# Kernel optimization log

Hardware: AMD Instinct MI355X
Metric: run time of the kernel (lower is better)

## Reference

```python
import jax, jax.numpy as jnp
import numpy as np

D_MODEL, D_EDGE, D_STRUCT = 128, 64, 8
N, E, B = 50000, 800000, 1

def _lin(key, din, dout):
    kw, kb = jax.random.split(key)
    s = 1.0 / np.sqrt(din)
    return (jax.random.uniform(kw, (din, dout), jnp.float32, -s, s),
            jax.random.uniform(kb, (dout,), jnp.float32, -s, s))

def setup_inputs() -> dict:
    key = jax.random.key(0)
    ks = jax.random.split(key, 16)
    H = jax.random.normal(ks[0], (B, N, D_MODEL), jnp.float32)
    xyz = jax.random.normal(ks[1], (B, N, 3), jnp.float32)
    edge_index = jax.random.randint(ks[2], (2, E), 0, N, jnp.int64)
    edge_struct = jax.random.normal(ks[3], (E, D_STRUCT), jnp.float32)
    edge_rest_lengths = jax.random.uniform(ks[4], (E,), jnp.float32)
    We1, be1 = _lin(ks[5], 2 * D_MODEL + 2 + D_STRUCT, D_EDGE)
    We2, be2 = _lin(ks[6], D_EDGE, D_EDGE)
    Wg1, bg1 = _lin(ks[7], 2 + D_STRUCT, 32)
    Wg2, bg2 = _lin(ks[8], 32, 1)
    Wn1, bn1 = _lin(ks[9], D_MODEL + D_EDGE, 2 * D_MODEL)
    Wn2, bn2 = _lin(ks[10], 2 * D_MODEL, D_MODEL)
    ln_g = jnp.ones((D_MODEL,), jnp.float32)
    ln_b = jnp.zeros((D_MODEL,), jnp.float32)
    return dict(H=H, xyz=xyz, edge_index=edge_index, edge_struct=edge_struct,
                edge_rest_lengths=edge_rest_lengths,
                We1=We1, be1=be1, We2=We2, be2=be2,
                Wg1=Wg1, bg1=bg1, Wg2=Wg2, bg2=bg2,
                Wn1=Wn1, bn1=bn1, Wn2=Wn2, bn2=bn2,
                ln_g=ln_g, ln_b=ln_b)

def reference(H, xyz, edge_index, edge_struct, edge_rest_lengths,
              We1, be1, We2, be2, Wg1, bg1, Wg2, bg2,
              Wn1, bn1, Wn2, bn2, ln_g, ln_b):
    Bn, Nn, d = H.shape
    i, j = edge_index[0], edge_index[1]
    # edge geometry
    diff = xyz[:, i, :] - xyz[:, j, :]                      # (B,E,3)
    dist2 = jnp.sum(diff * diff, axis=-1, keepdims=True)    # (B,E,1)
    dist = jnp.sqrt(dist2 + 1e-9)
    rest = edge_rest_lengths.reshape(1, -1, 1)
    delta = (dist - rest) / (rest + 1e-9)
    struct = jnp.broadcast_to(edge_struct[None], (Bn, edge_struct.shape[0], edge_struct.shape[1]))
    # edge message MLP
    Hi, Hj = H[:, i, :], H[:, j, :]
    e_in = jnp.concatenate([Hi, Hj, dist2, delta, struct], axis=-1)  # (B,E,2d+2+ds)
    e = jax.nn.silu(e_in @ We1 + be1)
    e_msg = jax.nn.silu(e @ We2 + be2)                       # (B,E,d_edge)
    # gate
    g_in = jnp.concatenate([dist2, delta, struct], axis=-1)
    g = jax.nn.sigmoid(jax.nn.silu(g_in @ Wg1 + bg1) @ Wg2 + bg2)  # (B,E,1)
    e_msg = e_msg * g
    # scatter-add aggregate to destination node i
    agg = jnp.zeros((Bn, Nn, e_msg.shape[-1]), H.dtype).at[:, i, :].add(e_msg)
    # node MLP (dropout is identity at eval) + residual + LayerNorm
    n_in = jnp.concatenate([H, agg], axis=-1)
    upd = jax.nn.silu(n_in @ Wn1 + bn1) @ Wn2 + bn2
    x = H + upd
    mu = jnp.mean(x, axis=-1, keepdims=True)
    var = jnp.mean((x - mu) ** 2, axis=-1, keepdims=True)
    return (x - mu) / jnp.sqrt(var + 1e-5) * ln_g + ln_b
```

## Files before the change

kernel.cpp:

```cpp
#include <hip/hip_runtime.h>
#include <stdint.h>

#define N_NODES 50000
#define N_EDGES 800000
#define NODE_TILES 782

#define SE   72
#define SW2  72
#define SPQ  136
#define SN1  216
#define SN2  280
#define ATS  40

#define EC_GRID 962
#define EC_CHUNK 13

#define SCAN_B 98

typedef short bf16x8 __attribute__((ext_vector_type(8)));
typedef short short4v __attribute__((ext_vector_type(4)));
typedef unsigned short ushort8 __attribute__((ext_vector_type(8)));
typedef unsigned int uint4v __attribute__((ext_vector_type(4)));
typedef float f32x4  __attribute__((ext_vector_type(4)));

static __device__ __forceinline__ unsigned short f2bf(float f) {
  unsigned int x = __float_as_uint(f);
  unsigned int r = (x + 0x7fffu + ((x >> 16) & 1u)) >> 16;
  return (unsigned short)r;
}
static __device__ __forceinline__ float bf2f(unsigned short u) {
  return __uint_as_float(((unsigned int)u) << 16);
}
static __device__ __forceinline__ float silu_f(float x) {
  return x * __builtin_amdgcn_rcpf(1.0f + __expf(-x));
}
static __device__ __forceinline__ float sigmoid_f(float x) {
  return __builtin_amdgcn_rcpf(1.0f + __expf(-x));
}
static __device__ __forceinline__ unsigned int cvt_pk_bf16(float lo, float hi) {
  unsigned int r;
  asm("v_cvt_pk_bf16_f32 %0, %1, %2" : "=v"(r) : "v"(lo), "v"(hi));
  return r;
}
static __device__ __forceinline__ bf16x8 pack8(float4 u, float4 v) {
  bf16x8 w;
  w[0] = (short)f2bf(u.x); w[1] = (short)f2bf(u.y);
  w[2] = (short)f2bf(u.z); w[3] = (short)f2bf(u.w);
  w[4] = (short)f2bf(v.x); w[5] = (short)f2bf(v.y);
  w[6] = (short)f2bf(v.z); w[7] = (short)f2bf(v.w);
  return w;
}

__global__ void prep_hist(
    const int* __restrict__ eidx,
    const float* __restrict__ We1, const float* __restrict__ be1,
    const float* __restrict__ We2,
    const float* __restrict__ Wn1, const float* __restrict__ Wn2,
    unsigned short* __restrict__ WpqT, unsigned short* __restrict__ We2T,
    unsigned short* __restrict__ Wn1T, unsigned short* __restrict__ Wn2T,
    unsigned short* __restrict__ WrT,
    int* __restrict__ cnt)
{
  const int gid = blockIdx.x * 256 + threadIdx.x;
  const int gsz = gridDim.x * 256;
  for (int i = gid; i < 128 * SPQ; i += gsz) {
    int n = i / SPQ, k = i % SPQ;
    unsigned short v = 0;
    if (k < 128) v = (n < 64) ? f2bf(We1[k * 64 + n]) : f2bf(We1[(128 + k) * 64 + (n - 64)]);
    WpqT[i] = v;
  }
  for (int i = gid; i < 64 * SW2; i += gsz) {
    int n = i / SW2, k = i % SW2;
    We2T[i] = (k < 64) ? f2bf(We2[k * 64 + n]) : (unsigned short)0;
  }
  for (int i = gid; i < 256 * SN1; i += gsz) {
    int n = i / SN1, k = i % SN1;
    Wn1T[i] = (k < 192) ? f2bf(Wn1[k * 256 + n]) : (unsigned short)0;
  }
  for (int i = gid; i < 128 * SN2; i += gsz) {
    int n = i / SN2, k = i % SN2;
    Wn2T[i] = (k < 256) ? f2bf(Wn2[k * 128 + n]) : (unsigned short)0;
  }
  for (int i = gid; i < 64 * 32; i += gsz) {
    int n = i >> 5, k = i & 31;
    float v = 0.f;
    if (k < 2)       v = We1[256 * 64 + n];
    else if (k < 4)  v = We1[257 * 64 + n];
    else if (k < 12) v = We1[(258 + (k - 4)) * 64 + n];
    else if (k == 12) v = be1[n];
    else if (k == 13) { float w = We1[256 * 64 + n]; v = w - bf2f(f2bf(w)); }
    else if (k == 14) { float w = We1[257 * 64 + n]; v = w - bf2f(f2bf(w)); }
    else if (k == 15) { float w = be1[n];            v = w - bf2f(f2bf(w)); }
    WrT[i] = (k < 16) ? f2bf(v) : (unsigned short)0;
  }
  if (gid < N_EDGES) atomicAdd(&cnt[eidx[gid]], 1);
}

__global__ __launch_bounds__(512) void scan_local(
    const int* __restrict__ cnt, int* __restrict__ rowptr,
    int* __restrict__ bsum)
{
  __shared__ int wsum[8], woff[8];
  const int t = threadIdx.x;
  const int idx = blockIdx.x * 512 + t;
  const int lane = t & 63, wid = t >> 6;
  int c = (idx < N_NODES) ? cnt[idx] : 0;
  int v = c;
  #pragma unroll
  for (int o = 1; o < 64; o <<= 1) {
    int u = __shfl_up(v, o);
    if (lane >= o) v += u;
  }
  if (lane == 63) wsum[wid] = v;
  __syncthreads();
  if (t == 0) {
    int a = 0;
    #pragma unroll
    for (int w = 0; w < 8; ++w) { woff[w] = a; a += wsum[w]; }
    bsum[blockIdx.x] = a;
  }
  __syncthreads();
  if (idx < N_NODES) rowptr[idx] = woff[wid] + (v - c);
}

__global__ __launch_bounds__(128) void scan_mid(
    const int* __restrict__ bsum, int* __restrict__ boff)
{
  __shared__ int ws[2];
  const int t = threadIdx.x;
  const int lane = t & 63, wid = t >> 6;
  int c = (t < SCAN_B) ? bsum[t] : 0;
  int v = c;
  #pragma unroll
  for (int o = 1; o < 64; o <<= 1) {
    int u = __shfl_up(v, o);
    if (lane >= o) v += u;
  }
  if (lane == 63) ws[wid] = v;
  __syncthreads();
  int add = (wid == 1) ? ws[0] : 0;
  if (t < SCAN_B) boff[t] = add + (v - c);
}

__global__ __launch_bounds__(512) void scan_add(
    const int* __restrict__ rowptr, const int* __restrict__ boff,
    int* __restrict__ cursor, float4* __restrict__ agg)
{
  const int idx = blockIdx.x * 512 + threadIdx.x;
  if (idx < N_NODES) cursor[idx] = rowptr[idx] + boff[blockIdx.x];
  if (idx < 50048) {
    float4 z = make_float4(0.f, 0.f, 0.f, 0.f);
    float4* p = agg + (long)idx * 16;
    #pragma unroll
    for (int k = 0; k < 16; ++k) p[k] = z;
  }
}

__global__ void fill_reorder(
    const int* __restrict__ eidx, const float* __restrict__ xyz,
    const float* __restrict__ estruct, const float* __restrict__ erest,
    int* __restrict__ cursor,
    const float* __restrict__ Wg1, const float* __restrict__ bg1,
    const float* __restrict__ Wg2, const float* __restrict__ bg2,
    unsigned short* __restrict__ rec)
{
  int e = blockIdx.x * 256 + threadIdx.x;
  if (e >= N_EDGES) return;
  int i = eidx[e], j = eidx[N_EDGES + e];
  float dx = xyz[i * 3 + 0] - xyz[j * 3 + 0];
  float dy = xyz[i * 3 + 1] - xyz[j * 3 + 1];
  float dz = xyz[i * 3 + 2] - xyz[j * 3 + 2];
  float d2 = dx * dx + dy * dy + dz * dz;
  float dist = sqrtf(d2 + 1e-9f);
  float rest = erest[e];
  float dl = (dist - rest) / (rest + 1e-9f);
  float4 s0 = *(const float4*)&estruct[e * 8];
  float4 s1 = *(const float4*)&estruct[e * 8 + 4];
  float st[8] = {s0.x, s0.y, s0.z, s0.w, s1.x, s1.y, s1.z, s1.w};
  float gsum = 0.f;
  #pragma unroll
  for (int h = 0; h < 32; ++h) {
    float a = bg1[h] + d2 * Wg1[0 * 32 + h] + dl * Wg1[1 * 32 + h];
    #pragma unroll
    for (int c = 0; c < 8; ++c) a += st[c] * Wg1[(2 + c) * 32 + h];
    gsum += silu_f(a) * Wg2[h];
  }
  float g = sigmoid_f(gsum + bg2[0]);

  unsigned short d2h = f2bf(d2);
  unsigned short d2l = f2bf(d2 - bf2f(d2h));
  unsigned short dlh = f2bf(dl);
  unsigned short dll = f2bf(dl - bf2f(dlh));

  ushort8 w0;
  w0[0] = d2h; w0[1] = d2l; w0[2] = dlh; w0[3] = dll;
  w0[4] = f2bf(st[0]); w0[5] = f2bf(st[1]); w0[6] = f2bf(st[2]); w0[7] = f2bf(st[3]);
  uint4v w1;
  w1[0] = (unsigned int)f2bf(st[4]) | ((unsigned int)f2bf(st[5]) << 16);
  w1[1] = (unsigned int)f2bf(st[6]) | ((unsigned int)f2bf(st[7]) << 16);
  w1[2] = __float_as_uint(g);
  w1[3] = (unsigned int)i | ((unsigned int)j << 16);

  int pos = atomicAdd(&cursor[i], 1);
  unsigned short* dst = rec + (long)pos * 16;
  *(uint4v*)dst = *(uint4v*)&w0;
  *(uint4v*)(dst + 8) = w1;
}

__global__ __launch_bounds__(256, 4) void pq_kernel(
    const float* __restrict__ H, const unsigned short* __restrict__ WpqT,
    unsigned short* __restrict__ P, unsigned short* __restrict__ Q,
    unsigned short* __restrict__ Hbf)
{
  __shared__ unsigned short Ws[128 * SPQ];

  const int tid  = threadIdx.x;
  const int lane = tid & 63;
  const int wv   = tid >> 6;
  const int lr   = lane & 15;
  const int lq   = lane >> 4;
  const int n0   = blockIdx.x * 64;
  const int m0   = wv * 16;

  for (int i = tid * 8; i < 128 * SPQ; i += 256 * 8)
    *(bf16x8*)&Ws[i] = *(const bf16x8*)&WpqT[i];
  __syncthreads();

  const int rowa = n0 + m0 + lr;
  const int rowc = rowa < N_NODES ? rowa : N_NODES - 1;

  f32x4 zero4 = {0.f, 0.f, 0.f, 0.f};
  f32x4 acc[8];
  #pragma unroll
  for (int f = 0; f < 8; ++f) acc[f] = zero4;

  #pragma unroll
  for (int s = 0; s < 4; ++s) {
    int kb = s * 32 + lq * 8;
    const float* p = H + (long)rowc * 128 + kb;
    float4 u = *(const float4*)p;
    float4 v = *(const float4*)(p + 4);
    bf16x8 a = pack8(u, v);
    *(bf16x8*)&Hbf[(long)rowa * 128 + kb] = a;
    #pragma unroll
    for (int f = 0; f < 8; ++f) {
      bf16x8 b = *(const bf16x8*)&Ws[(f * 16 + lr) * SPQ + kb];
      acc[f] = __builtin_amdgcn_mfma_f32_16x16x32_bf16(a, b, acc[f], 0, 0, 0);
    }
  }
  #pragma unroll
  for (int f = 0; f < 8; ++f) {
    #pragma unroll
    for (int r = 0; r < 4; ++r) {
      int node = n0 + m0 + lq * 4 + r;
      if (node < N_NODES) {
        if (f < 4) P[(long)node * 64 + f * 16 + lr] = f2bf(acc[f][r]);
        else       Q[(long)node * 64 + (f - 4) * 16 + lr] = f2bf(acc[f][r]);
      }
    }
  }
}

__global__ __launch_bounds__(256, 4) void edge_compute(
    const unsigned short* __restrict__ P, const unsigned short* __restrict__ Q,
    const unsigned short* __restrict__ rec,
    const unsigned short* __restrict__ We2T, const float* __restrict__ be2,
    const unsigned short* __restrict__ WrT,
    float* __restrict__ agg)
{
  __shared__ unsigned short W2s[64 * SW2];
  __shared__ unsigned short Es [4 * 16 * SE];
  __shared__ unsigned short At [4 * 16 * ATS];

  const int tid  = threadIdx.x;
  const int lane = tid & 63;
  const int wv   = tid >> 6;
  const int lr   = lane & 15;
  const int lq   = lane >> 4;

  for (int i = tid * 8; i < 64 * SW2; i += 256 * 8)
    *(bf16x8*)&W2s[i] = *(const bf16x8*)&We2T[i];

  unsigned short* Es_w = &Es[wv * 16 * SE];
  unsigned short* At_w = &At[wv * 16 * ATS];

  if (lane < 16) {
    ushort8 z;
    #pragma unroll
    for (int c = 0; c < 8; ++c) z[c] = 0;
    *(ushort8*)&At_w[lane * ATS + 16] = z;
    *(ushort8*)&At_w[lane * ATS + 24] = z;
  }

  bf16x8 aWr[4];
  float bias2[4][4];
  #pragma unroll
  for (int f = 0; f < 4; ++f) {
    aWr[f] = *(const bf16x8*)&WrT[(f * 16 + lr) * 32 + lq * 8];
    #pragma unroll
    for (int r = 0; r < 4; ++r) bias2[f][r] = be2[f * 16 + lq * 4 + r];
  }
  __syncthreads();

  const int n_tiles = N_EDGES / 16;
  const int wid = blockIdx.x * 4 + wv;
  const int t0 = wid * EC_CHUNK;
  const int t1 = (t0 + EC_CHUNK < n_tiles) ? (t0 + EC_CHUNK) : n_tiles;
  if (t0 >= n_tiles) return;

  f32x4 zero4 = {0.f, 0.f, 0.f, 0.f};
  int   cur_node;
  {
    int ij0 = *(const int*)(rec + (long)t0 * 16 * 16 + 14);
    cur_node = ij0 & 0xffff;
  }
  float acc        = 0.f;
  bool  use_atomic = true;

  for (int tile = t0; tile < t1; ++tile) {
    const int s0 = tile * 16;

    const unsigned short* rp = rec + (long)(s0 + lr) * 16;
    ushort8 ra = *(const ushort8*)rp;
    uint4   rb = *(const uint4*)(rp + 8);
    float g     = __uint_as_float(rb.z);
    int   inode = (int)(rb.w & 0xffff);
    int   jnode = (int)((rb.w >> 16) & 0xffff);

    if (lane < 16) {
      ushort8 w1;
      w1[0] = (unsigned short)(rb.x & 0xffff);
      w1[1] = (unsigned short)(rb.x >> 16);
      w1[2] = (unsigned short)(rb.y & 0xffff);
      w1[3] = (unsigned short)(rb.y >> 16);
      w1[4] = 0x3F80u; w1[5] = (unsigned short)ra[0];
      w1[6] = (unsigned short)ra[2]; w1[7] = 0x3F80u;
      *(ushort8*)&At_w[lane * ATS]     = ra;
      *(ushort8*)&At_w[lane * ATS + 8] = w1;
    }

    bf16x8 bA = *(const bf16x8*)&At_w[lr * ATS + lq * 8];
    f32x4 acc1[4];
    #pragma unroll
    for (int f = 0; f < 4; ++f)
      acc1[f] = __builtin_amdgcn_mfma_f32_16x16x32_bf16(aWr[f], bA, zero4, 0, 0, 0);

    const unsigned short* Pb = P + (long)inode * 64;
    const unsigned short* Qb = Q + (long)jnode * 64;
    #pragma unroll
    for (int f = 0; f < 4; ++f) {
      short4v pv = *(const short4v*)&Pb[f * 16 + lq * 4];
      short4v qv = *(const short4v*)&Qb[f * 16 + lq * 4];
      float v0 = silu_f(bf2f((unsigned short)pv[0]) + bf2f((unsigned short)qv[0]) + acc1[f][0]);
      float v1 = silu_f(bf2f((unsigned short)pv[1]) + bf2f((unsigned short)qv[1]) + acc1[f][1]);
      float v2 = silu_f(bf2f((unsigned short)pv[2]) + bf2f((unsigned short)qv[2]) + acc1[f][2]);
      float v3 = silu_f(bf2f((unsigned short)pv[3]) + bf2f((unsigned short)qv[3]) + acc1[f][3]);
      uint2 w;
      w.x = cvt_pk_bf16(v0, v1);
      w.y = cvt_pk_bf16(v2, v3);
      *(uint2*)&Es_w[lr * SE + f * 16 + lq * 4] = w;
    }

    f32x4 acc2[4];
    #pragma unroll
    for (int f = 0; f < 4; ++f) acc2[f] = zero4;
    #pragma unroll
    for (int s = 0; s < 2; ++s) {
      int kb = s * 32 + lq * 8;
      bf16x8 bE = *(const bf16x8*)&Es_w[lr * SE + kb];
      #pragma unroll
      for (int f = 0; f < 4; ++f) {
        bf16x8 aW = *(const bf16x8*)&W2s[(f * 16 + lr) * SW2 + kb];
        acc2[f] = __builtin_amdgcn_mfma_f32_16x16x32_bf16(aW, bE, acc2[f], 0, 0, 0);
      }
    }

    #pragma unroll
    for (int f = 0; f < 4; ++f) {
      float o0 = silu_f(acc2[f][0] + bias2[f][0]) * g;
      float o1 = silu_f(acc2[f][1] + bias2[f][1]) * g;
      float o2 = silu_f(acc2[f][2] + bias2[f][2]) * g;
      float o3 = silu_f(acc2[f][3] + bias2[f][3]) * g;
      uint2 w;
      w.x = cvt_pk_bf16(o0, o1);
      w.y = cvt_pk_bf16(o2, o3);
      *(uint2*)&Es_w[lr * SE + f * 16 + lq * 4] = w;
    }

    float mv[16];
    #pragma unroll
    for (int e = 0; e < 16; ++e) mv[e] = bf2f(Es_w[e * SE + lane]);

    int up = __shfl_up(inode, 1);
    unsigned long long bm = __ballot(inode != up);
    unsigned mask = (unsigned)bm & 0xFFFEu;
    int i0 = __builtin_amdgcn_readlane(inode, 0);
    if (i0 != cur_node) mask |= 1u;

    #pragma unroll
    for (int e = 0; e < 16; ++e) {
      if (mask & (1u << e)) {
        if (use_atomic) atomicAdd(&agg[(long)cur_node * 64 + lane], acc);
        else            agg[(long)cur_node * 64 + lane] = acc;
        use_atomic = false;
        cur_node = __builtin_amdgcn_readlane(inode, e);
        acc = 0.f;
      }
      acc += mv[e];
    }
  }
  atomicAdd(&agg[(long)cur_node * 64 + lane], acc);
}

__global__ __launch_bounds__(256, 2) void h1_kernel(
    const unsigned short* __restrict__ Hbf, const float* __restrict__ agg,
    const unsigned short* __restrict__ Wn1T, const float* __restrict__ bn1,
    unsigned short* __restrict__ h1)
{
  __shared__ unsigned short Wl[128 * SN1];

  const int tid  = threadIdx.x;
  const int lane = tid & 63;
  const int wv   = tid >> 6;
  const int lr   = lane & 15;
  const int lq   = lane >> 4;
  const int m0   = wv * 16;
  const int p    = blockIdx.x & 1;

  for (int i = tid * 8; i < 128 * SN1; i += 256 * 8)
    *(bf16x8*)&Wl[i] = *(const bf16x8*)&Wn1T[p * 128 * SN1 + i];
  __syncthreads();

  f32x4 zero4 = {0.f, 0.f, 0.f, 0.f};
  for (int t = blockIdx.x >> 1; t < NODE_TILES; t += 256) {
    const int n0 = t * 64;
    int rowa = n0 + m0 + lr;
    int rowc = rowa < N_NODES ? rowa : N_NODES - 1;

    f32x4 acc1[8];
    #pragma unroll
    for (int f = 0; f < 8; ++f) acc1[f] = zero4;
    #pragma unroll
    for (int s = 0; s < 6; ++s) {
      int kb = s * 32 + lq * 8;
      bf16x8 a;
      if (s < 4) {
        a = *(const bf16x8*)&Hbf[(long)rowa * 128 + kb];
      } else {
        const float* pp = agg + (long)rowc * 64 + (kb - 128);
        float4 u = *(const float4*)pp;
        float4 v = *(const float4*)(pp + 4);
        a = pack8(u, v);
      }
      #pragma unroll
      for (int f = 0; f < 8; ++f) {
        bf16x8 b = *(const bf16x8*)&Wl[(f * 16 + lr) * SN1 + kb];
        acc1[f] = __builtin_amdgcn_mfma_f32_16x16x32_bf16(a, b, acc1[f], 0, 0, 0);
      }
    }
    #pragma unroll
    for (int f = 0; f < 8; ++f) {
      int col = p * 128 + f * 16 + lr;
      float bias = bn1[col];
      #pragma unroll
      for (int r = 0; r < 4; ++r) {
        int node = n0 + m0 + lq * 4 + r;
        h1[(long)node * 256 + col] = f2bf(silu_f(acc1[f][r] + bias));
      }
    }
  }
}

__global__ __launch_bounds__(256, 2) void out_kernel(
    const float* __restrict__ H, const unsigned short* __restrict__ h1,
    const unsigned short* __restrict__ Wn2T, const float* __restrict__ bn2,
    const float* __restrict__ ln_g, const float* __restrict__ ln_b,
    float* __restrict__ out)
{
  __shared__ unsigned short Wl[128 * SN2];

  const int tid  = threadIdx.x;
  const int lane = tid & 63;
  const int wv   = tid >> 6;
  const int lr   = lane & 15;
  const int lq   = lane >> 4;
  const int m0   = wv * 16;

  for (int i = tid * 8; i < 128 * SN2; i += 256 * 8)
    *(bf16x8*)&Wl[i] = *(const bf16x8*)&Wn2T[i];
  __syncthreads();

  f32x4 zero4 = {0.f, 0.f, 0.f, 0.f};
  for (int t = blockIdx.x; t < NODE_TILES; t += 512) {
    const int n0 = t * 64;
    int rowa = n0 + m0 + lr;

    f32x4 acc2[8];
    #pragma unroll
    for (int f = 0; f < 8; ++f) acc2[f] = zero4;
    #pragma unroll
    for (int s = 0; s < 8; ++s) {
      int kb = s * 32 + lq * 8;
      bf16x8 a = *(const bf16x8*)&h1[(long)rowa * 256 + kb];
      #pragma unroll
      for (int f = 0; f < 8; ++f) {
        bf16x8 b = *(const bf16x8*)&Wl[(f * 16 + lr) * SN2 + kb];
        acc2[f] = __builtin_amdgcn_mfma_f32_16x16x32_bf16(a, b, acc2[f], 0, 0, 0);
      }
    }

    #pragma unroll
    for (int r = 0; r < 4; ++r) {
      int node = n0 + m0 + lq * 4 + r;
      int nc = node < N_NODES ? node : N_NODES - 1;
      float x[8];
      float sum = 0.f, sumsq = 0.f;
      #pragma unroll
      for (int f = 0; f < 8; ++f) {
        int n = f * 16 + lr;
        float u = acc2[f][r] + bn2[n];
        float xv = H[(long)nc * 128 + n] + u;
        x[f] = xv;
        sum += xv;
        sumsq += xv * xv;
      }
      #pragma unroll
      for (int o = 1; o < 16; o <<= 1) {
        sum   += __shfl_xor(sum, o);
        sumsq += __shfl_xor(sumsq, o);
      }
      float mu  = sum * (1.f / 128.f);
      float var = sumsq * (1.f / 128.f) - mu * mu;
      float rstd = rsqrtf(var + 1e-5f);
      if (node < N_NODES) {
        #pragma unroll
        for (int f = 0; f < 8; ++f) {
          int n = f * 16 + lr;
          out[(long)node * 128 + n] = (x[f] - mu) * rstd * ln_g[n] + ln_b[n];
        }
      }
    }
  }
}

extern "C" void kernel_launch(void* const* d_in, const int* in_sizes, int n_in,
                              void* d_out, int out_size, void* d_ws, size_t ws_size,
                              hipStream_t stream) {
  const float* H       = (const float*)d_in[0];
  const float* xyz     = (const float*)d_in[1];
  const int*   eidx    = (const int*)d_in[2];
  const float* estruct = (const float*)d_in[3];
  const float* erest   = (const float*)d_in[4];
  const float* We1     = (const float*)d_in[5];
  const float* be1     = (const float*)d_in[6];
  const float* We2     = (const float*)d_in[7];
  const float* be2     = (const float*)d_in[8];
  const float* Wg1     = (const float*)d_in[9];
  const float* bg1     = (const float*)d_in[10];
  const float* Wg2     = (const float*)d_in[11];
  const float* bg2     = (const float*)d_in[12];
  const float* Wn1     = (const float*)d_in[13];
  const float* bn1     = (const float*)d_in[14];
  const float* Wn2     = (const float*)d_in[15];
  const float* bn2     = (const float*)d_in[16];
  const float* ln_g    = (const float*)d_in[17];
  const float* ln_b    = (const float*)d_in[18];

  char* ws = (char*)d_ws;
  float*          agg    = (float*)(ws + 0);
  unsigned short* Hbf    = (unsigned short*)(ws + 12812288);
  unsigned short* rec    = (unsigned short*)(ws + 25624576);
  unsigned short* P      = (unsigned short*)(ws + 51224576);
  unsigned short* Qm     = (unsigned short*)(ws + 57624576);
  int*            cnt    = (int*)(ws + 64024576);
  int*            rowptr = (int*)(ws + 64224768);
  int*            cursor = (int*)(ws + 64424960);
  unsigned short* WpqT   = (unsigned short*)(ws + 64625152);
  unsigned short* We2T   = (unsigned short*)(ws + 64659968);
  unsigned short* Wn1T   = (unsigned short*)(ws + 64669184);
  unsigned short* Wn2T   = (unsigned short*)(ws + 64779776);
  unsigned short* WrT    = (unsigned short*)(ws + 64851456);
  int*            bsum   = (int*)(ws + 64855552);
  int*            boff   = (int*)(ws + 64856064);
  unsigned short* h1     = (unsigned short*)(ws + 64856576);
  float* out = (float*)d_out;

  hipMemsetAsync(cnt, 0, (size_t)N_NODES * sizeof(int), stream);

  hipLaunchKernelGGL(prep_hist, dim3(3125), dim3(256), 0, stream,
                     eidx, We1, be1, We2, Wn1, Wn2, WpqT, We2T, Wn1T, Wn2T, WrT, cnt);
  hipLaunchKernelGGL(scan_local, dim3(SCAN_B), dim3(512), 0, stream,
                     cnt, rowptr, bsum);
  hipLaunchKernelGGL(scan_mid, dim3(1), dim3(128), 0, stream,
                     bsum, boff);
  hipLaunchKernelGGL(scan_add, dim3(SCAN_B), dim3(512), 0, stream,
                     rowptr, boff, cursor, (float4*)agg);
  hipLaunchKernelGGL(fill_reorder, dim3(3125), dim3(256), 0, stream,
                     eidx, xyz, estruct, erest, cursor,
                     Wg1, bg1, Wg2, bg2, rec);
  hipLaunchKernelGGL(pq_kernel, dim3(NODE_TILES), dim3(256), 0, stream,
                     H, WpqT, P, Qm, Hbf);
  hipLaunchKernelGGL(edge_compute, dim3(EC_GRID), dim3(256), 0, stream,
                     P, Qm, rec, We2T, be2, WrT, agg);
  hipLaunchKernelGGL(h1_kernel, dim3(512), dim3(256), 0, stream,
                     Hbf, agg, Wn1T, bn1, h1);
  hipLaunchKernelGGL(out_kernel, dim3(512), dim3(256), 0, stream,
                     H, h1, Wn2T, bn2, ln_g, ln_b, out);
}
```

Measured before the change: 362.3 us.

## Drop CSR sort and fuse edge geometry and gate MLP into edge kernel

Removes the histogram, three-phase scan and reorder pass that sorted edges by destination node. Edge geometry, features and the gate MLP (now run on MFMA with bf16 weights) are computed inside the edge kernel. Aggregation switches from segmented register reduction to per-element float atomicAdd into agg. This removes several launches and the write and read of the 25 MB record buffer, but issues 64 atomics per edge to random nodes (about 51M atomics) and computes the gate in bf16, which loses precision.

```diff
diff --git a/kernel.cpp b/kernel.cpp
--- a/kernel.cpp
+++ b/kernel.cpp
@@ -14,8 +14,6 @@
 
 #define EC_GRID 962
 #define EC_CHUNK 13
-
-#define SCAN_B 98
 
 typedef short bf16x8 __attribute__((ext_vector_type(8)));
 typedef short short4v __attribute__((ext_vector_type(4)));
@@ -51,15 +49,14 @@
   return w;
 }
 
-__global__ void prep_hist(
-    const int* __restrict__ eidx,
+__global__ void prep_w(
     const float* __restrict__ We1, const float* __restrict__ be1,
     const float* __restrict__ We2,
     const float* __restrict__ Wn1, const float* __restrict__ Wn2,
+    const float* __restrict__ Wg1, const float* __restrict__ bg1,
     unsigned short* __restrict__ WpqT, unsigned short* __restrict__ We2T,
     unsigned short* __restrict__ Wn1T, unsigned short* __restrict__ Wn2T,
-    unsigned short* __restrict__ WrT,
-    int* __restrict__ cnt)
+    unsigned short* __restrict__ WrT,  unsigned short* __restrict__ WgT)
 {
   const int gid = blockIdx.x * 256 + threadIdx.x;
   const int gsz = gridDim.x * 256;
@@ -93,118 +90,15 @@
     else if (k == 15) { float w = be1[n];            v = w - bf2f(f2bf(w)); }
     WrT[i] = (k < 16) ? f2bf(v) : (unsigned short)0;
   }
-  if (gid < N_EDGES) atomicAdd(&cnt[eidx[gid]], 1);
-}
-
-__global__ __launch_bounds__(512) void scan_local(
-    const int* __restrict__ cnt, int* __restrict__ rowptr,
-    int* __restrict__ bsum)
-{
-  __shared__ int wsum[8], woff[8];
-  const int t = threadIdx.x;
-  const int idx = blockIdx.x * 512 + t;
-  const int lane = t & 63, wid = t >> 6;
-  int c = (idx < N_NODES) ? cnt[idx] : 0;
-  int v = c;
-  #pragma unroll
-  for (int o = 1; o < 64; o <<= 1) {
-    int u = __shfl_up(v, o);
-    if (lane >= o) v += u;
-  }
-  if (lane == 63) wsum[wid] = v;
-  __syncthreads();
-  if (t == 0) {
-    int a = 0;
-    #pragma unroll
-    for (int w = 0; w < 8; ++w) { woff[w] = a; a += wsum[w]; }
-    bsum[blockIdx.x] = a;
-  }
-  __syncthreads();
-  if (idx < N_NODES) rowptr[idx] = woff[wid] + (v - c);
-}
-
-__global__ __launch_bounds__(128) void scan_mid(
-    const int* __restrict__ bsum, int* __restrict__ boff)
-{
-  __shared__ int ws[2];
-  const int t = threadIdx.x;
-  const int lane = t & 63, wid = t >> 6;
-  int c = (t < SCAN_B) ? bsum[t] : 0;
-  int v = c;
-  #pragma unroll
-  for (int o = 1; o < 64; o <<= 1) {
-    int u = __shfl_up(v, o);
-    if (lane >= o) v += u;
-  }
-  if (lane == 63) ws[wid] = v;
-  __syncthreads();
-  int add = (wid == 1) ? ws[0] : 0;
-  if (t < SCAN_B) boff[t] = add + (v - c);
-}
-
-__global__ __launch_bounds__(512) void scan_add(
-    const int* __restrict__ rowptr, const int* __restrict__ boff,
-    int* __restrict__ cursor, float4* __restrict__ agg)
-{
-  const int idx = blockIdx.x * 512 + threadIdx.x;
-  if (idx < N_NODES) cursor[idx] = rowptr[idx] + boff[blockIdx.x];
-  if (idx < 50048) {
-    float4 z = make_float4(0.f, 0.f, 0.f, 0.f);
-    float4* p = agg + (long)idx * 16;
-    #pragma unroll
-    for (int k = 0; k < 16; ++k) p[k] = z;
-  }
-}
-
-__global__ void fill_reorder(
-    const int* __restrict__ eidx, const float* __restrict__ xyz,
-    const float* __restrict__ estruct, const float* __restrict__ erest,
-    int* __restrict__ cursor,
-    const float* __restrict__ Wg1, const float* __restrict__ bg1,
-    const float* __restrict__ Wg2, const float* __restrict__ bg2,
-    unsigned short* __restrict__ rec)
-{
-  int e = blockIdx.x * 256 + threadIdx.x;
-  if (e >= N_EDGES) return;
-  int i = eidx[e], j = eidx[N_EDGES + e];
-  float dx = xyz[i * 3 + 0] - xyz[j * 3 + 0];
-  float dy = xyz[i * 3 + 1] - xyz[j * 3 + 1];
-  float dz = xyz[i * 3 + 2] - xyz[j * 3 + 2];
-  float d2 = dx * dx + dy * dy + dz * dz;
-  float dist = sqrtf(d2 + 1e-9f);
-  float rest = erest[e];
-  float dl = (dist - rest) / (rest + 1e-9f);
-  float4 s0 = *(const float4*)&estruct[e * 8];
-  float4 s1 = *(const float4*)&estruct[e * 8 + 4];
-  float st[8] = {s0.x, s0.y, s0.z, s0.w, s1.x, s1.y, s1.z, s1.w};
-  float gsum = 0.f;
-  #pragma unroll
-  for (int h = 0; h < 32; ++h) {
-    float a = bg1[h] + d2 * Wg1[0 * 32 + h] + dl * Wg1[1 * 32 + h];
-    #pragma unroll
-    for (int c = 0; c < 8; ++c) a += st[c] * Wg1[(2 + c) * 32 + h];
-    gsum += silu_f(a) * Wg2[h];
-  }
-  float g = sigmoid_f(gsum + bg2[0]);
-
-  unsigned short d2h = f2bf(d2);
-  unsigned short d2l = f2bf(d2 - bf2f(d2h));
-  unsigned short dlh = f2bf(dl);
-  unsigned short dll = f2bf(dl - bf2f(dlh));
-
-  ushort8 w0;
-  w0[0] = d2h; w0[1] = d2l; w0[2] = dlh; w0[3] = dll;
-  w0[4] = f2bf(st[0]); w0[5] = f2bf(st[1]); w0[6] = f2bf(st[2]); w0[7] = f2bf(st[3]);
-  uint4v w1;
-  w1[0] = (unsigned int)f2bf(st[4]) | ((unsigned int)f2bf(st[5]) << 16);
-  w1[1] = (unsigned int)f2bf(st[6]) | ((unsigned int)f2bf(st[7]) << 16);
-  w1[2] = __float_as_uint(g);
-  w1[3] = (unsigned int)i | ((unsigned int)j << 16);
-
-  int pos = atomicAdd(&cursor[i], 1);
-  unsigned short* dst = rec + (long)pos * 16;
-  *(uint4v*)dst = *(uint4v*)&w0;
-  *(uint4v*)(dst + 8) = w1;
+  for (int i = gid; i < 32 * 32; i += gsz) {
+    int h = i >> 5, k = i & 31;
+    float v = 0.f;
+    if (k < 2)       v = Wg1[0 * 32 + h];
+    else if (k < 4)  v = Wg1[1 * 32 + h];
+    else if (k < 12) v = Wg1[(2 + (k - 4)) * 32 + h];
+    else if (k == 12) v = bg1[h];
+    WgT[i] = f2bf(v);
+  }
 }
 
 __global__ __launch_bounds__(256, 4) void pq_kernel(
@@ -261,11 +155,13 @@
   }
 }
 
-__global__ __launch_bounds__(256, 4) void edge_compute(
+__global__ __launch_bounds__(256, 4) void edge_all(
+    const int* __restrict__ eidx, const float* __restrict__ xyz,
+    const float* __restrict__ estruct, const float* __restrict__ erest,
     const unsigned short* __restrict__ P, const unsigned short* __restrict__ Q,
-    const unsigned short* __restrict__ rec,
     const unsigned short* __restrict__ We2T, const float* __restrict__ be2,
-    const unsigned short* __restrict__ WrT,
+    const unsigned short* __restrict__ WrT, const unsigned short* __restrict__ WgT,
+    const float* __restrict__ Wg2, const float* __restrict__ bg2,
     float* __restrict__ agg)
 {
   __shared__ unsigned short W2s[64 * SW2];
@@ -292,14 +188,21 @@
     *(ushort8*)&At_w[lane * ATS + 24] = z;
   }
 
-  bf16x8 aWr[4];
-  float bias2[4][4];
+  bf16x8 aWr[4], aWg[2];
+  float bias2[4][4], wg2v[2][4];
   #pragma unroll
   for (int f = 0; f < 4; ++f) {
     aWr[f] = *(const bf16x8*)&WrT[(f * 16 + lr) * 32 + lq * 8];
     #pragma unroll
     for (int r = 0; r < 4; ++r) bias2[f][r] = be2[f * 16 + lq * 4 + r];
   }
+  #pragma unroll
+  for (int hb = 0; hb < 2; ++hb) {
+    aWg[hb] = *(const bf16x8*)&WgT[(hb * 16 + lr) * 32 + lq * 8];
+    #pragma unroll
+    for (int r = 0; r < 4; ++r) wg2v[hb][r] = Wg2[hb * 16 + lq * 4 + r];
+  }
+  const float bg2s = bg2[0];
   __syncthreads();
 
   const int n_tiles = N_EDGES / 16;
@@ -309,37 +212,51 @@
   if (t0 >= n_tiles) return;
 
   f32x4 zero4 = {0.f, 0.f, 0.f, 0.f};
-  int   cur_node;
-  {
-    int ij0 = *(const int*)(rec + (long)t0 * 16 * 16 + 14);
-    cur_node = ij0 & 0xffff;
-  }
-  float acc        = 0.f;
-  bool  use_atomic = true;
 
   for (int tile = t0; tile < t1; ++tile) {
     const int s0 = tile * 16;
 
-    const unsigned short* rp = rec + (long)(s0 + lr) * 16;
-    ushort8 ra = *(const ushort8*)rp;
-    uint4   rb = *(const uint4*)(rp + 8);
-    float g     = __uint_as_float(rb.z);
-    int   inode = (int)(rb.w & 0xffff);
-    int   jnode = (int)((rb.w >> 16) & 0xffff);
-
+    int iN = 0, jN = 0;
     if (lane < 16) {
-      ushort8 w1;
-      w1[0] = (unsigned short)(rb.x & 0xffff);
-      w1[1] = (unsigned short)(rb.x >> 16);
-      w1[2] = (unsigned short)(rb.y & 0xffff);
-      w1[3] = (unsigned short)(rb.y >> 16);
-      w1[4] = 0x3F80u; w1[5] = (unsigned short)ra[0];
-      w1[6] = (unsigned short)ra[2]; w1[7] = 0x3F80u;
-      *(ushort8*)&At_w[lane * ATS]     = ra;
+      int e = s0 + lane;
+      iN = eidx[e];
+      jN = eidx[N_EDGES + e];
+      float rest = erest[e];
+      float4 sa = *(const float4*)&estruct[(long)e * 8];
+      float4 sb = *(const float4*)&estruct[(long)e * 8 + 4];
+      float dx = xyz[iN * 3 + 0] - xyz[jN * 3 + 0];
+      float dy = xyz[iN * 3 + 1] - xyz[jN * 3 + 1];
+      float dz = xyz[iN * 3 + 2] - xyz[jN * 3 + 2];
+      float d2 = dx * dx + dy * dy + dz * dz;
+      float dist = sqrtf(d2 + 1e-9f);
+      float dl = (dist - rest) / (rest + 1e-9f);
+      unsigned short d2h = f2bf(d2);
+      unsigned short d2l = f2bf(d2 - bf2f(d2h));
+      unsigned short dlh = f2bf(dl);
+      unsigned short dll = f2bf(dl - bf2f(dlh));
+      ushort8 w0, w1;
+      w0[0] = d2h; w0[1] = d2l; w0[2] = dlh; w0[3] = dll;
+      w0[4] = f2bf(sa.x); w0[5] = f2bf(sa.y); w0[6] = f2bf(sa.z); w0[7] = f2bf(sa.w);
+      w1[0] = f2bf(sb.x); w1[1] = f2bf(sb.y); w1[2] = f2bf(sb.z); w1[3] = f2bf(sb.w);
+      w1[4] = 0x3F80u; w1[5] = d2h; w1[6] = dlh; w1[7] = 0x3F80u;
+      *(ushort8*)&At_w[lane * ATS]     = w0;
       *(ushort8*)&At_w[lane * ATS + 8] = w1;
     }
+    int inode = __shfl(iN, lr);
+    int jnode = __shfl(jN, lr);
 
     bf16x8 bA = *(const bf16x8*)&At_w[lr * ATS + lq * 8];
+
+    f32x4 ag0 = __builtin_amdgcn_mfma_f32_16x16x32_bf16(aWg[0], bA, zero4, 0, 0, 0);
+    f32x4 ag1 = __builtin_amdgcn_mfma_f32_16x16x32_bf16(aWg[1], bA, zero4, 0, 0, 0);
+    float gp = 0.f;
+    #pragma unroll
+    for (int r = 0; r < 4; ++r)
+      gp += silu_f(ag0[r]) * wg2v[0][r] + silu_f(ag1[r]) * wg2v[1][r];
+    gp += __shfl_xor(gp, 16);
+    gp += __shfl_xor(gp, 32);
+    float g = sigmoid_f(gp + bg2s);
+
     f32x4 acc1[4];
     #pragma unroll
     for (int f = 0; f < 4; ++f)
@@ -375,41 +292,19 @@
       }
     }
 
+    float* ap = agg + (long)inode * 64;
     #pragma unroll
     for (int f = 0; f < 4; ++f) {
       float o0 = silu_f(acc2[f][0] + bias2[f][0]) * g;
       float o1 = silu_f(acc2[f][1] + bias2[f][1]) * g;
       float o2 = silu_f(acc2[f][2] + bias2[f][2]) * g;
       float o3 = silu_f(acc2[f][3] + bias2[f][3]) * g;
-      uint2 w;
-      w.x = cvt_pk_bf16(o0, o1);
-      w.y = cvt_pk_bf16(o2, o3);
-      *(uint2*)&Es_w[lr * SE + f * 16 + lq * 4] = w;
-    }
-
-    float mv[16];
-    #pragma unroll
-    for (int e = 0; e < 16; ++e) mv[e] = bf2f(Es_w[e * SE + lane]);
-
-    int up = __shfl_up(inode, 1);
-    unsigned long long bm = __ballot(inode != up);
-    unsigned mask = (unsigned)bm & 0xFFFEu;
-    int i0 = __builtin_amdgcn_readlane(inode, 0);
-    if (i0 != cur_node) mask |= 1u;
-
-    #pragma unroll
-    for (int e = 0; e < 16; ++e) {
-      if (mask & (1u << e)) {
-        if (use_atomic) atomicAdd(&agg[(long)cur_node * 64 + lane], acc);
-        else            agg[(long)cur_node * 64 + lane] = acc;
-        use_atomic = false;
-        cur_node = __builtin_amdgcn_readlane(inode, e);
-        acc = 0.f;
-      }
-      acc += mv[e];
-    }
-  }
-  atomicAdd(&agg[(long)cur_node * 64 + lane], acc);
+      atomicAdd(&ap[f * 16 + lq * 4 + 0], o0);
+      atomicAdd(&ap[f * 16 + lq * 4 + 1], o1);
+      atomicAdd(&ap[f * 16 + lq * 4 + 2], o2);
+      atomicAdd(&ap[f * 16 + lq * 4 + 3], o3);
+    }
+  }
 }
 
 __global__ __launch_bounds__(256, 2) void h1_kernel(
@@ -569,39 +464,27 @@
   char* ws = (char*)d_ws;
   float*          agg    = (float*)(ws + 0);
   unsigned short* Hbf    = (unsigned short*)(ws + 12812288);
-  unsigned short* rec    = (unsigned short*)(ws + 25624576);
-  unsigned short* P      = (unsigned short*)(ws + 51224576);
-  unsigned short* Qm     = (unsigned short*)(ws + 57624576);
-  int*            cnt    = (int*)(ws + 64024576);
-  int*            rowptr = (int*)(ws + 64224768);
-  int*            cursor = (int*)(ws + 64424960);
-  unsigned short* WpqT   = (unsigned short*)(ws + 64625152);
-  unsigned short* We2T   = (unsigned short*)(ws + 64659968);
-  unsigned short* Wn1T   = (unsigned short*)(ws + 64669184);
-  unsigned short* Wn2T   = (unsigned short*)(ws + 64779776);
-  unsigned short* WrT    = (unsigned short*)(ws + 64851456);
-  int*            bsum   = (int*)(ws + 64855552);
-  int*            boff   = (int*)(ws + 64856064);
-  unsigned short* h1     = (unsigned short*)(ws + 64856576);
+  unsigned short* P      = (unsigned short*)(ws + 25624576);
+  unsigned short* Qm     = (unsigned short*)(ws + 32024576);
+  unsigned short* WpqT   = (unsigned short*)(ws + 38424576);
+  unsigned short* We2T   = (unsigned short*)(ws + 38459392);
+  unsigned short* Wn1T   = (unsigned short*)(ws + 38468608);
+  unsigned short* Wn2T   = (unsigned short*)(ws + 38579200);
+  unsigned short* WrT    = (unsigned short*)(ws + 38650880);
+  unsigned short* WgT    = (unsigned short*)(ws + 38654976);
+  unsigned short* h1     = (unsigned short*)(ws + 38657024);
   float* out = (float*)d_out;
 
-  hipMemsetAsync(cnt, 0, (size_t)N_NODES * sizeof(int), stream);
-
-  hipLaunchKernelGGL(prep_hist, dim3(3125), dim3(256), 0, stream,
-                     eidx, We1, be1, We2, Wn1, Wn2, WpqT, We2T, Wn1T, Wn2T, WrT, cnt);
-  hipLaunchKernelGGL(scan_local, dim3(SCAN_B), dim3(512), 0, stream,
-                     cnt, rowptr, bsum);
-  hipLaunchKernelGGL(scan_mid, dim3(1), dim3(128), 0, stream,
-                     bsum, boff);
-  hipLaunchKernelGGL(scan_add, dim3(SCAN_B), dim3(512), 0, stream,
-                     rowptr, boff, cursor, (float4*)agg);
-  hipLaunchKernelGGL(fill_reorder, dim3(3125), dim3(256), 0, stream,
-                     eidx, xyz, estruct, erest, cursor,
-                     Wg1, bg1, Wg2, bg2, rec);
+  hipMemsetAsync(agg, 0, (size_t)50048 * 64 * sizeof(float), stream);
+
+  hipLaunchKernelGGL(prep_w, dim3(512), dim3(256), 0, stream,
+                     We1, be1, We2, Wn1, Wn2, Wg1, bg1,
+                     WpqT, We2T, Wn1T, Wn2T, WrT, WgT);
   hipLaunchKernelGGL(pq_kernel, dim3(NODE_TILES), dim3(256), 0, stream,
                      H, WpqT, P, Qm, Hbf);
-  hipLaunchKernelGGL(edge_compute, dim3(EC_GRID), dim3(256), 0, stream,
-                     P, Qm, rec, We2T, be2, WrT, agg);
+  hipLaunchKernelGGL(edge_all, dim3(EC_GRID), dim3(256), 0, stream,
+                     eidx, xyz, estruct, erest, P, Qm,
+                     We2T, be2, WrT, WgT, Wg2, bg2, agg);
   hipLaunchKernelGGL(h1_kernel, dim3(512), dim3(256), 0, stream,
                      Hbf, agg, Wn1T, bn1, h1);
   hipLaunchKernelGGL(out_kernel, dim3(512), dim3(256), 0, stream,
```

New measurement: 886.8 us. +144.8%, slower.
